# Kernel tuning notes

Hardware: AMD Instinct MI355X
Metric: run time of the kernel (lower is better)

The kernel has to match this reference:

```python
import jax, jax.numpy as jnp
import numpy as np

B, C, H, W, L, R = 1, 32, 96, 128, 2, 3
N = 2 * R + 1
EPS = 1e-5


def conv2d(x, w, stride=1, pad=1):
    return jax.lax.conv_general_dilated(
        x, w, (stride, stride), ((pad, pad), (pad, pad)),
        dimension_numbers=('NCHW', 'OIHW', 'NCHW'))


def conv_transpose2d(x, w, stride=2, pad=1):
    # torch ConvTranspose2d semantics; w: [Cin, Cout, kH, kW]
    kh, kw = w.shape[2], w.shape[3]
    wf = jnp.flip(w, (2, 3)).transpose(1, 0, 2, 3)  # [Cout, Cin, kh, kw]
    return jax.lax.conv_general_dilated(
        x, wf, (1, 1),
        ((kh - 1 - pad, kh - 1 - pad), (kw - 1 - pad, kw - 1 - pad)),
        lhs_dilation=(stride, stride),
        dimension_numbers=('NCHW', 'OIHW', 'NCHW'))


def bnorm(x, s, b, m, v):
    # inference-mode BatchNorm2d (fixed running stats)
    inv = s * jax.lax.rsqrt(v + EPS)
    return x * inv[None, :, None, None] + (b - m * inv)[None, :, None, None]


def grid_sample(img, grid):
    # bilinear, align_corners=True, padding_mode='zeros'
    # img [B,C,H,W], grid [B,Hg,Wg,2] (x,y) in [-1,1]
    Bi, Ci, Hi, Wi = img.shape
    gx = (grid[..., 0] + 1.0) * 0.5 * (Wi - 1)
    gy = (grid[..., 1] + 1.0) * 0.5 * (Hi - 1)
    x0 = jnp.floor(gx)
    y0 = jnp.floor(gy)
    wx = (gx - x0)[:, None]  # [B,1,Hg,Wg]
    wy = (gy - y0)[:, None]

    def tap(yf, xf):
        valid = (xf >= 0) & (xf <= Wi - 1) & (yf >= 0) & (yf <= Hi - 1)
        xc = jnp.clip(xf, 0, Wi - 1).astype(jnp.int32)
        yc = jnp.clip(yf, 0, Hi - 1).astype(jnp.int32)
        v = jax.vmap(lambda im, y, x: im[:, y, x])(img, yc, xc)  # [B,C,Hg,Wg]
        return v * valid[:, None].astype(img.dtype)

    v00 = tap(y0, x0)
    v01 = tap(y0, x0 + 1)
    v10 = tap(y0 + 1, x0)
    v11 = tap(y0 + 1, x0 + 1)
    return (v00 * (1 - wx) * (1 - wy) + v01 * wx * (1 - wy)
            + v10 * (1 - wx) * wy + v11 * wx * wy)


def _forward(fmap1_0, fmap1_1, fmap2_0, fmap2_1, coords,
             cw1, cw2, cw3, cw4, ctw5, cw6, cb6,
             bn1s, bn1b, bn1m, bn1v, bn2s, bn2b, bn2m, bn2v,
             bn3s, bn3b, bn3m, bn3v, bn4s, bn4b, bn4m, bn4v,
             bn5s, bn5b, bn5m, bn5v, dap_w):
    n = N
    dx = jnp.linspace(-R, R, n)
    delta = jnp.stack(jnp.meshgrid(dx, dx, indexing='ij'), axis=-1)  # [n,n,2]
    b, _, h, w = coords.shape
    cp = coords.transpose(0, 2, 3, 1)  # [b,h,w,2] (x,y)
    bns = ((bn1s, bn1b, bn1m, bn1v), (bn2s, bn2b, bn2m, bn2v),
           (bn3s, bn3b, bn3m, bn3v), (bn4s, bn4b, bn4m, bn4v),
           (bn5s, bn5b, bn5m, bn5v))
    out = []
    for i, (f1, f2) in enumerate(((fmap1_0, fmap2_0), (fmap1_1, fmap2_1))):
        c, h2, w2 = f1.shape[1], f1.shape[2], f1.shape[3]
        # [b,n,h,n,w,2]: first n axis pairs with h, second with w (as in torch view)
        cent = cp[:, None, :, None, :, :] / (2.0 ** i) + delta[None, :, None, :, None, :]
        gx = 2.0 * cent[..., 0] / (w2 - 1) - 1.0
        gy = 2.0 * cent[..., 1] / (h2 - 1) - 1.0
        grid = jnp.stack([gx, gy], -1).reshape(b, n * h, n * w, 2)
        f2s = grid_sample(f2, grid).reshape(b, c, n, h, n, w)
        f2s = f2s.transpose(0, 2, 4, 1, 3, 5)  # [b,du,dv,c,h,w]
        f1e = jnp.broadcast_to(f1[:, None, None], (b, n, n, c, h, w))
        x = jnp.concatenate([f1e, f2s], axis=3).reshape(b * n * n, 2 * c, h, w)
        # MatchingNet (DICL): conv-bn-relu stack, stride-2 down + transposed up
        x = jax.nn.relu(bnorm(conv2d(x, cw1[i]), *(p[i] for p in bns[0])))
        x = jax.nn.relu(bnorm(conv2d(x, cw2[i], stride=2), *(p[i] for p in bns[1])))
        x = jax.nn.relu(bnorm(conv2d(x, cw3[i]), *(p[i] for p in bns[2])))
        x = jax.nn.relu(bnorm(conv2d(x, cw4[i]), *(p[i] for p in bns[3])))
        x = jax.nn.relu(bnorm(conv_transpose2d(x, ctw5[i]), *(p[i] for p in bns[4])))
        x = conv2d(x, cw6[i]) + cb6[i][None, :, None, None]  # [b*n*n,1,h,w]
        cost = x.reshape(b, n * n, h, w)
        # DisplacementAwareProjection: 1x1 conv over the 49 displacement channels
        cost = jnp.einsum('pq,bqhw->bphw', dap_w[i], cost)
        out.append(cost)
    return jnp.concatenate(out, axis=1)  # [b, L*(2r+1)^2, h, w]


def setup_inputs():
    key = jax.random.key(0)
    ks = jax.random.split(key, 40)

    def rn(k, shape, scale=1.0):
        return jax.random.normal(k, shape, jnp.float32) * scale

    inp = {}
    inp['fmap1_0'] = rn(ks[0], (B, C, H, W))
    inp['fmap2_0'] = rn(ks[1], (B, C, H, W))
    inp['fmap1_1'] = rn(ks[2], (B, C, H, W))
    inp['fmap2_1'] = rn(ks[3], (B, C, H, W))
    gy, gx = jnp.meshgrid(jnp.arange(H, dtype=jnp.float32),
                          jnp.arange(W, dtype=jnp.float32), indexing='ij')
    base = jnp.stack([gx, gy], 0)[None]  # [1,2,H,W] (x,y) pixel coords
    inp['coords'] = base + rn(ks[4], (B, 2, H, W), 2.0)

    def cw(k, co, ci, kk):
        return rn(k, (L, co, ci, kk, kk), 1.0 / np.sqrt(ci * kk * kk))

    inp['cw1'] = cw(ks[5], 96, 2 * C, 3)
    inp['cw2'] = cw(ks[6], 128, 96, 3)
    inp['cw3'] = cw(ks[7], 128, 128, 3)
    inp['cw4'] = cw(ks[8], 64, 128, 3)
    inp['ctw5'] = rn(ks[9], (L, 64, 32, 4, 4), 1.0 / np.sqrt(64 * 16))
    inp['cw6'] = cw(ks[10], 1, 32, 3)
    inp['cb6'] = rn(ks[11], (L, 1), 0.1)
    for j, ch in enumerate((96, 128, 128, 64, 32), start=1):
        k4 = jax.random.split(ks[11 + j], 4)
        inp['bn%ds' % j] = 1.0 + rn(k4[0], (L, ch), 0.1)
        inp['bn%db' % j] = rn(k4[1], (L, ch), 0.1)
        inp['bn%dm' % j] = rn(k4[2], (L, ch), 0.1)
        inp['bn%dv' % j] = 1.0 + rn(k4[3], (L, ch), 0.1) ** 2
    # DAP identity init
    inp['dap_w'] = jnp.tile(jnp.eye(N * N, dtype=jnp.float32)[None], (L, 1, 1))
    return inp


def reference(fmap1_0, fmap1_1, fmap2_0, fmap2_1, coords,
              cw1, cw2, cw3, cw4, ctw5, cw6, cb6,
              bn1s, bn1b, bn1m, bn1v, bn2s, bn2b, bn2m, bn2v,
              bn3s, bn3b, bn3m, bn3v, bn4s, bn4b, bn4m, bn4v,
              bn5s, bn5b, bn5m, bn5v, dap_w):
    return _forward(fmap1_0, fmap1_1, fmap2_0, fmap2_1, coords,
                    cw1, cw2, cw3, cw4, ctw5, cw6, cb6,
                    bn1s, bn1b, bn1m, bn1v, bn2s, bn2b, bn2m, bn2v,
                    bn3s, bn3b, bn3m, bn3v, bn4s, bn4b, bn4m, bn4v,
                    bn5s, bn5b, bn5m, bn5v, dap_w)
```

## Files before the change

### kernel.cpp

```cpp
#include <hip/hip_runtime.h>

#define EPSF 1e-5f

typedef __attribute__((ext_vector_type(8))) short short8;
typedef __attribute__((ext_vector_type(4))) float f32x4;

__device__ __forceinline__ ushort f2bf(float x) {
    union { float f; unsigned u; } c; c.f = x;
    unsigned r = c.u + 0x7FFF + ((c.u >> 16) & 1);
    return (ushort)(r >> 16);
}
__device__ __forceinline__ float bf2f(ushort b) {
    union { unsigned u; float f; } c; c.u = ((unsigned)b) << 16;
    return c.f;
}
__device__ __forceinline__ int swz(int a) {
    return a ^ (((a >> 7) & 7) << 4);
}


__global__ __launch_bounds__(256) void k_repack_conv(
    const float* __restrict__ src, ushort* __restrict__ dst, int CO, int CI)
{
    int idx = blockIdx.x * 256 + threadIdx.x;
    if (idx >= CO * CI * 9) return;
    int co = idx / (CI * 9);
    int rem = idx % (CI * 9);
    int ci = rem / 9, tap = rem % 9;
    dst[((size_t)tap * CO + co) * CI + ci] = f2bf(src[idx]);
}

__global__ __launch_bounds__(256) void k_repack_ct(
    const float* __restrict__ src, ushort* __restrict__ dst)
{
    int idx = blockIdx.x * 256 + threadIdx.x;
    if (idx >= 4 * 4 * 32 * 64) return;
    int ci = idx & 63;
    int t = idx >> 6;
    int co = t & 31; t >>= 5;
    int tap = t & 3;
    int parity = t >> 2;
    int ph = parity >> 1, pw = parity & 1;
    int a = tap >> 1, b = tap & 1;
    int kh = ((ph + 1) & 1) + 2 * a;
    int kw = ((pw + 1) & 1) + 2 * b;
    dst[idx] = f2bf(src[((ci * 32 + co) * 4 + kh) * 4 + kw]);
}

__global__ __launch_bounds__(256) void k_pack_f1(
    const float* __restrict__ f1_0, const float* __restrict__ f1_1,
    ushort* __restrict__ xf1)
{
    const int sp = blockIdx.x * 256 + threadIdx.x;
    const int l = blockIdx.z;
    const float* f1 = l ? f1_1 : f1_0;
    ushort* dst = xf1 + (size_t)l * 393216 + (size_t)sp * 32;
    #pragma unroll
    for (int g = 0; g < 4; ++g) {
        uint4 pk;
        uint* pw_ = (uint*)&pk;
        #pragma unroll
        for (int q = 0; q < 4; ++q) {
            int c = g * 8 + q * 2;
            pw_[q] = (uint)f2bf(f1[(size_t)c * 12288 + sp])
                   | ((uint)f2bf(f1[(size_t)(c + 1) * 12288 + sp]) << 16);
        }
        *(uint4*)(dst + g * 8) = pk;
    }
}

__global__ __launch_bounds__(256) void k_sample_nhwc(
    const float* __restrict__ f2_0, const float* __restrict__ f2_1,
    const float* __restrict__ coords, ushort* __restrict__ x0s, int d0)
{
    const int HW = 12288;
    const int sp = blockIdx.x * 256 + threadIdx.x;
    const int slot = blockIdx.z;
    const int p = d0 + slot;
    const int l = p / 49;
    const int d = p - l * 49;
    const int du = d / 7, dv = d % 7;
    const float inv_scale = l ? 0.5f : 1.0f;
    const float* f2 = l ? f2_1 : f2_0;

    float cx = coords[sp] * inv_scale + (float)(du - 3);
    float cy = coords[HW + sp] * inv_scale + (float)(dv - 3);
    float xf = floorf(cx), yf = floorf(cy);
    float wx = cx - xf, wy = cy - yf;
    int xi = (int)xf, yi = (int)yf;
    float vx0 = (xf >= 0.f && xf <= 127.f) ? 1.f : 0.f;
    float vx1 = (xf + 1.f >= 0.f && xf + 1.f <= 127.f) ? 1.f : 0.f;
    float vy0 = (yf >= 0.f && yf <= 95.f) ? 1.f : 0.f;
    float vy1 = (yf + 1.f >= 0.f && yf + 1.f <= 95.f) ? 1.f : 0.f;
    int x0i = min(max(xi, 0), 127), x1i = min(max(xi + 1, 0), 127);
    int y0i = min(max(yi, 0), 95),  y1i = min(max(yi + 1, 0), 95);
    float w00 = (1.f - wx) * (1.f - wy) * vx0 * vy0;
    float w01 = wx * (1.f - wy) * vx1 * vy0;
    float w10 = (1.f - wx) * wy * vx0 * vy1;
    float w11 = wx * wy * vx1 * vy1;
    int o00 = y0i * 128 + x0i, o01 = y0i * 128 + x1i;
    int o10 = y1i * 128 + x0i, o11 = y1i * 128 + x1i;

    ushort* dst = x0s + ((size_t)slot * HW + sp) * 32;
    #pragma unroll
    for (int g = 0; g < 4; ++g) {
        uint4 pk;
        uint* pw_ = (uint*)&pk;
        #pragma unroll
        for (int q = 0; q < 4; ++q) {
            uint wv = 0;
            #pragma unroll
            for (int h = 0; h < 2; ++h) {
                int c = g * 8 + q * 2 + h;
                const float* fc = f2 + (size_t)c * HW;
                float s = w00 * fc[o00] + w01 * fc[o01] + w10 * fc[o10] + w11 * fc[o11];
                wv |= ((uint)f2bf(s)) << (16 * h);
            }
            pw_[q] = wv;
        }
        *(uint4*)(dst + g * 8) = pk;
    }
}

template <int EPI>
__global__ __launch_bounds__(512, 2) void k_conv1(
    const ushort* __restrict__ in,
    ushort* __restrict__ out,
    const ushort* __restrict__ wbase,
    const float* __restrict__ p1,
    const float* __restrict__ bs0, const float* __restrict__ bb0,
    const float* __restrict__ bm0, const float* __restrict__ bv0,
    int d0, int koff)
{
    constexpr int AB = 10 * 66 * 64;
    constexpr int PB = 3 * 48 * 64;
    constexpr int SA = 6;
    __shared__ __align__(16) char smem[AB + 2 * PB];
    char* As = smem;

    const int tid = threadIdx.x;
    const int lane = tid & 63, wid = tid >> 6;
    const int lr = lane & 15, kg = lane >> 4;
    const int bx = blockIdx.x;
    const int rt = bx >> 1, ct = bx & 1;
    const int r0 = rt * 8, c0 = ct * 64;
    const int y = blockIdx.y;
    const int co0 = y * 48;
    const int slot = blockIdx.z;
    const int l = EPI ? slot : (d0 + slot) / 49;

    const ushort* ib = in + (size_t)slot * 12288 * 32;
    const ushort* wl = wbase + (size_t)l * (9 * 96 * 64);
    const short8 z8 = {0, 0, 0, 0, 0, 0, 0, 0};

    #pragma unroll
    for (int i = 0; i < SA; ++i) {
        int lin = i * 8192 + tid * 16;
        if (lin < AB) {
            int pos = lin >> 6;
            int prow = (pos * 994) >> 16;
            int pcol = pos - prow * 66;
            int grow = r0 - 1 + prow, gcol = c0 - 1 + pcol;
            bool ok = ((unsigned)grow < 96u) && ((unsigned)gcol < 128u);
            short8 v = z8;
            if (ok) v = *(const short8*)(ib + (grow * 128 + gcol) * 32 + ((lin & 63) >> 1));
            *(short8*)(As + swz(lin)) = v;
        }
    }

    int boff[2]; unsigned bmask = 0;
    #pragma unroll
    for (int i = 0; i < 2; ++i) {
        int lin = i * 8192 + tid * 16;
        if (lin < PB) bmask |= 1u << i;
        int lc = min(lin, PB - 16);
        int rowidx = lc >> 6;
        int tpg = rowidx / 48;
        int r = rowidx - tpg * 48;
        boff[i] = (tpg * 96 + co0 + r) * 64 + koff + ((lc & 63) >> 1);
    }
    short8 stgB[2];
    auto loadB = [&](int pg) {
        const ushort* src = wl + pg * (3 * 96 * 64);
        #pragma unroll
        for (int i = 0; i < 2; ++i)
            if ((bmask >> i) & 1) stgB[i] = *(const short8*)(src + boff[i]);
    };
    auto writeB = [&](int pg) {
        char* Bs = smem + AB + (pg & 1) * PB;
        #pragma unroll
        for (int i = 0; i < 2; ++i) {
            int lin = i * 8192 + tid * 16;
            if ((bmask >> i) & 1) *(short8*)(Bs + swz(lin)) = stgB[i];
        }
    };

    f32x4 acc[4][3];
    if constexpr (EPI == 0) {
        const float* pl = p1 + (size_t)l * 1179648
                        + ((size_t)((bx * 2 + y) * 512 + tid)) * 48;
        #pragma unroll
        for (int mf = 0; mf < 4; ++mf)
            #pragma unroll
            for (int nf = 0; nf < 3; ++nf)
                acc[mf][nf] = *(const f32x4*)(pl + (mf * 3 + nf) * 4);
    } else {
        #pragma unroll
        for (int mf = 0; mf < 4; ++mf)
            #pragma unroll
            for (int nf = 0; nf < 3; ++nf)
                acc[mf][nf] = (f32x4){0.f, 0.f, 0.f, 0.f};
    }

    loadB(0);
    writeB(0);
    __syncthreads();

    #pragma unroll
    for (int ps = 0; ps < 3; ++ps) {
        if (ps < 2) loadB(ps + 1);
        const char* Bs = smem + AB + (ps & 1) * PB;
        #pragma unroll
        for (int kw = 0; kw < 3; ++kw) {
            short8 a[4];
            #pragma unroll
            for (int mf = 0; mf < 4; ++mf) {
                int sp = (wid + ps) * 66 + mf * 16 + lr + kw;
                a[mf] = *(const short8*)(As + swz(sp * 64 + kg * 16));
            }
            #pragma unroll
            for (int nf = 0; nf < 3; ++nf) {
                short8 b = *(const short8*)(Bs + swz((kw * 48 + nf * 16 + lr) * 64 + kg * 16));
                #pragma unroll
                for (int mf = 0; mf < 4; ++mf)
                    acc[mf][nf] = __builtin_amdgcn_mfma_f32_16x16x32_bf16(
                        a[mf], b, acc[mf][nf], 0, 0, 0);
            }
        }
        __syncthreads();
        if (ps < 2) { writeB(ps + 1); __syncthreads(); }
    }

    if constexpr (EPI == 1) {
        float* of = (float*)out + (size_t)l * 1179648
                  + ((size_t)((bx * 2 + y) * 512 + tid)) * 48;
        #pragma unroll
        for (int mf = 0; mf < 4; ++mf)
            #pragma unroll
            for (int nf = 0; nf < 3; ++nf)
                *(f32x4*)(of + (mf * 3 + nf) * 4) = acc[mf][nf];
    } else {
        const float* bs = bs0 + l * 96;
        const float* bb = bb0 + l * 96;
        const float* bm = bm0 + l * 96;
        const float* bv = bv0 + l * 96;
        ushort* ob = out + (size_t)slot * 12288 * 96;
        const int orow = r0 + wid;
        #pragma unroll
        for (int nf = 0; nf < 3; ++nf) {
            const int col = co0 + nf * 16 + lr;
            const float inv = bs[col] * rsqrtf(bv[col] + EPSF);
            const float beta = bb[col] - bm[col] * inv;
            #pragma unroll
            for (int mf = 0; mf < 4; ++mf) {
                #pragma unroll
                for (int j = 0; j < 4; ++j) {
                    int ocol = c0 + mf * 16 + kg * 4 + j;
                    float yv = fmaxf(fmaf(acc[mf][nf][j], inv, beta), 0.f);
                    ob[((size_t)orow * 128 + ocol) * 96 + col] = f2bf(yv);
                }
            }
        }
    }
}

template <int CIN, int COUT, int IH, int IW>
__global__ __launch_bounds__(512, 4) void k_conv_lds8s(
    const ushort* __restrict__ in, ushort* __restrict__ out,
    const ushort* __restrict__ wbase, int wlstride,
    const float* __restrict__ bs0, const float* __restrict__ bb0,
    const float* __restrict__ bm0, const float* __restrict__ bv0, int d0)
{
    constexpr int CCs = CIN / 32;
    constexpr int AB = 10 * 66 * 64;
    constexpr int PB = 3 * 64 * 64;
    constexpr int SA = 6, SB = 2;
    constexpr int NPH = 3 * CCs;
    __shared__ __align__(16) char smem[AB + 2 * PB];
    char* As = smem;

    const int tid = threadIdx.x;
    const int lane = tid & 63, wid = tid >> 6;
    const int lr = lane & 15, kg = lane >> 4;
    const int r0 = (int)blockIdx.x * 8;
    const int co0 = (int)blockIdx.y * 64;
    const int slot = blockIdx.z;
    const int l = (d0 + slot) / 49;

    int aoff[SA]; unsigned awr = 0, avalid = 0;
    #pragma unroll
    for (int i = 0; i < SA; ++i) {
        int lin = i * 8192 + tid * 16;
        bool wr = lin < AB;
        int linc = wr ? lin : 0;
        int pos = linc >> 6;
        int prow = (pos * 994) >> 16;
        int pcol = pos - prow * 66;
        int grow = r0 - 1 + prow, gcol = pcol - 1;
        bool ok = wr && ((unsigned)grow < (unsigned)IH) && ((unsigned)gcol < (unsigned)IW);
        if (wr) awr |= 1u << i;
        if (ok) avalid |= 1u << i;
        int growc = min(max(grow, 0), IH - 1), gcolc = min(max(gcol, 0), IW - 1);
        aoff[i] = (growc * IW + gcolc) * CIN + ((linc & 63) >> 1);
    }
    int boff[SB]; unsigned bmask = 0;
    #pragma unroll
    for (int i = 0; i < SB; ++i) {
        int lin = i * 8192 + tid * 16;
        if (lin < PB) bmask |= 1u << i;
        int lc = min(lin, PB - 16);
        int rowidx = lc >> 6;
        int tpg = rowidx >> 6, r = rowidx & 63;
        boff[i] = (tpg * COUT + co0 + r) * CIN + ((lc & 63) >> 1);
    }

    const ushort* ib = in + (size_t)slot * IH * IW * CIN;
    const ushort* wl = wbase + (size_t)l * wlstride;
    const short8 z8 = {0, 0, 0, 0, 0, 0, 0, 0};

    auto stageA = [&](int cc) {
        #pragma unroll
        for (int i = 0; i < SA; ++i) {
            int lin = i * 8192 + tid * 16;
            if ((awr >> i) & 1) {
                short8 v = z8;
                if ((avalid >> i) & 1)
                    v = *(const short8*)(ib + aoff[i] + cc * 32);
                *(short8*)(As + swz(lin)) = v;
            }
        }
    };
    short8 stgB[SB];
    auto loadB = [&](int ps) {
        int pg = ps % 3, cc = ps / 3;
        const ushort* src = wl + pg * (3 * COUT * CIN) + cc * 32;
        #pragma unroll
        for (int i = 0; i < SB; ++i)
            if ((bmask >> i) & 1) stgB[i] = *(const short8*)(src + boff[i]);
    };
    auto writeB = [&](int ps) {
        char* Bs = smem + AB + (ps & 1) * PB;
        #pragma unroll
        for (int i = 0; i < SB; ++i) {
            int lin = i * 8192 + tid * 16;
            if ((bmask >> i) & 1) *(short8*)(Bs + swz(lin)) = stgB[i];
        }
    };

    f32x4 acc[4][4];
    #pragma unroll
    for (int mf = 0; mf < 4; ++mf)
        #pragma unroll
        for (int nf = 0; nf < 4; ++nf)
            acc[mf][nf] = (f32x4){0.f, 0.f, 0.f, 0.f};

    stageA(0);
    loadB(0); writeB(0);
    __syncthreads();

    #pragma unroll 1
    for (int ps = 0; ps < NPH; ++ps) {
        const int pg = ps % 3;
        const bool hasNext = (ps + 1 < NPH);
        if (hasNext) loadB(ps + 1);

        const char* Bs = smem + AB + (ps & 1) * PB;
        #pragma unroll
        for (int kw = 0; kw < 3; ++kw) {
            short8 a[4];
            #pragma unroll
            for (int mf = 0; mf < 4; ++mf) {
                int sp = (wid + pg) * 66 + mf * 16 + lr + kw;
                a[mf] = *(const short8*)(As + swz(sp * 64 + kg * 16));
            }
            #pragma unroll
            for (int nf = 0; nf < 4; ++nf) {
                short8 b = *(const short8*)(Bs + swz((kw * 64 + nf * 16 + lr) * 64 + kg * 16));
                #pragma unroll
                for (int mf = 0; mf < 4; ++mf)
                    acc[mf][nf] = __builtin_amdgcn_mfma_f32_16x16x32_bf16(
                        a[mf], b, acc[mf][nf], 0, 0, 0);
            }
        }

        __syncthreads();
        if (hasNext) {
            writeB(ps + 1);
            if (pg == 2) stageA(ps / 3 + 1);
            __syncthreads();
        }
    }

    const float* bs = bs0 + l * COUT;
    const float* bb = bb0 + l * COUT;
    const float* bm = bm0 + l * COUT;
    const float* bv = bv0 + l * COUT;
    ushort* ob = out + (size_t)slot * IH * IW * COUT;
    const int orow = r0 + wid;
    #pragma unroll
    for (int nf = 0; nf < 4; ++nf) {
        const int col = co0 + nf * 16 + lr;
        const float inv = bs[col] * rsqrtf(bv[col] + EPSF);
        const float beta = bb[col] - bm[col] * inv;
        #pragma unroll
        for (int mf = 0; mf < 4; ++mf) {
            #pragma unroll
            for (int j = 0; j < 4; ++j) {
                int ocol = mf * 16 + kg * 4 + j;
                float y = fmaxf(fmaf(acc[mf][nf][j], inv, beta), 0.f);
                ob[((size_t)orow * IW + ocol) * COUT + col] = f2bf(y);
            }
        }
    }
}

__global__ __launch_bounds__(512, 2) void k_conv_s2_8(
    const ushort* __restrict__ in, ushort* __restrict__ out,
    const ushort* __restrict__ wbase, int wlstride,
    const float* __restrict__ bs0, const float* __restrict__ bb0,
    const float* __restrict__ bm0, const float* __restrict__ bv0, int d0)
{
    constexpr int AB = 9 * 66 * 64;
    constexpr int PB = 3 * 64 * 64;
    constexpr int SA = 5;
    constexpr int SB = 2;
    constexpr int NPH = 9;
    __shared__ __align__(16) char smem[AB + 2 * PB];
    char* As = smem;

    const int tid = threadIdx.x;
    const int lane = tid & 63, wid = tid >> 6;
    const int lr = lane & 15, kg = lane >> 4;
    const int mw = wid >> 1, ch = wid & 1;
    const int bx = blockIdx.x;
    const int rt = bx >> 1, ct = bx & 1;
    const int r0 = rt * 4, oc0 = ct * 32;
    const int co0 = blockIdx.y * 64;
    const int slot = blockIdx.z;
    const int l = (d0 + slot) / 49;

    int aoff[SA]; unsigned awr = 0, avalid = 0;
    #pragma unroll
    for (int i = 0; i < SA; ++i) {
        int lin = i * 8192 + tid * 16;
        bool wr = lin < AB;
        int linc = wr ? lin : 0;
        int pos = linc >> 6;
        int prow = (pos * 994) >> 16;
        int pcol = pos - prow * 66;
        int grow = 2 * r0 - 1 + prow, gcol = 2 * oc0 - 1 + pcol;
        bool ok = wr && ((unsigned)grow < 96u) && ((unsigned)gcol < 128u);
        if (wr) awr |= 1u << i;
        if (ok) avalid |= 1u << i;
        int growc = min(max(grow, 0), 95), gcolc = min(max(gcol, 0), 127);
        aoff[i] = (growc * 128 + gcolc) * 96 + ((linc & 63) >> 1);
    }
    int boff[SB]; unsigned bmask = 0;
    #pragma unroll
    for (int i = 0; i < SB; ++i) {
        int lin = i * 8192 + tid * 16;
        if (lin < PB) bmask |= 1u << i;
        int lc = min(lin, PB - 16);
        int rowidx = lc >> 6;
        int tpg = rowidx >> 6, r = rowidx & 63;
        boff[i] = (tpg * 128 + co0 + r) * 96 + ((lc & 63) >> 1);
    }

    const ushort* ib = in + (size_t)slot * 12288 * 96;
    const ushort* wl = wbase + (size_t)l * wlstride;
    const short8 z8 = {0, 0, 0, 0, 0, 0, 0, 0};

    short8 stgA[SA], stgB[SB];
    auto loadA = [&](int cc) {
        #pragma unroll
        for (int i = 0; i < SA; ++i) {
            if ((avalid >> i) & 1) stgA[i] = *(const short8*)(ib + aoff[i] + cc * 32);
            else stgA[i] = z8;
        }
    };
    auto writeA = [&]() {
        #pragma unroll
        for (int i = 0; i < SA; ++i) {
            int lin = i * 8192 + tid * 16;
            if ((awr >> i) & 1)
                *(short8*)(As + swz(lin)) = stgA[i];
        }
    };
    auto loadB = [&](int ps) {
        int pg = ps % 3, cc = ps / 3;
        const ushort* src = wl + pg * (3 * 128 * 96) + cc * 32;
        #pragma unroll
        for (int i = 0; i < SB; ++i)
            if ((bmask >> i) & 1) stgB[i] = *(const short8*)(src + boff[i]);
    };
    auto writeB = [&](int ps) {
        char* Bs = smem + AB + (ps & 1) * PB;
        #pragma unroll
        for (int i = 0; i < SB; ++i) {
            int lin = i * 8192 + tid * 16;
            if ((bmask >> i) & 1)
                *(short8*)(Bs + swz(lin)) = stgB[i];
        }
    };

    f32x4 acc[2][2];
    #pragma unroll
    for (int mf = 0; mf < 2; ++mf)
        #pragma unroll
        for (int nf = 0; nf < 2; ++nf)
            acc[mf][nf] = (f32x4){0.f, 0.f, 0.f, 0.f};

    loadA(0); loadB(0);
    writeA(); writeB(0);
    __syncthreads();

    #pragma unroll 1
    for (int ps = 0; ps < NPH; ++ps) {
        const int pg = ps % 3;
        const bool hasNext = (ps + 1 < NPH);
        const bool newA = (pg == 2) && hasNext;
        if (hasNext) loadB(ps + 1);
        if (newA) loadA(ps / 3 + 1);

        const char* Bs = smem + AB + (ps & 1) * PB;
        #pragma unroll
        for (int kw = 0; kw < 3; ++kw) {
            short8 a[2];
            #pragma unroll
            for (int mf = 0; mf < 2; ++mf) {
                int pos = (2 * mw + pg) * 66 + 2 * (mf * 16 + lr) + kw;
                a[mf] = *(const short8*)(As + swz(pos * 64 + kg * 16));
            }
            #pragma unroll
            for (int nf = 0; nf < 2; ++nf) {
                int rb = kw * 64 + ch * 32 + nf * 16 + lr;
                short8 b = *(const short8*)(Bs + swz(rb * 64 + kg * 16));
                #pragma unroll
                for (int mf = 0; mf < 2; ++mf)
                    acc[mf][nf] = __builtin_amdgcn_mfma_f32_16x16x32_bf16(
                        a[mf], b, acc[mf][nf], 0, 0, 0);
            }
        }

        __syncthreads();
        if (hasNext) writeB(ps + 1);
        if (newA) writeA();
        if (hasNext) __syncthreads();
    }

    const float* bs = bs0 + l * 128;
    const float* bb = bb0 + l * 128;
    const float* bm = bm0 + l * 128;
    const float* bv = bv0 + l * 128;
    ushort* ob = out + (size_t)slot * 3072 * 128;
    const int orow = r0 + mw;
    #pragma unroll
    for (int nf = 0; nf < 2; ++nf) {
        const int col = co0 + ch * 32 + nf * 16 + lr;
        const float inv = bs[col] * rsqrtf(bv[col] + EPSF);
        const float beta = bb[col] - bm[col] * inv;
        #pragma unroll
        for (int mf = 0; mf < 2; ++mf) {
            #pragma unroll
            for (int j = 0; j < 4; ++j) {
                int ocol = oc0 + mf * 16 + kg * 4 + j;
                float y = fmaxf(fmaf(acc[mf][nf][j], inv, beta), 0.f);
                ob[((size_t)orow * 64 + ocol) * 128 + col] = f2bf(y);
            }
        }
    }
}

__global__ __launch_bounds__(256) void k_convt_mfma(
    const ushort* __restrict__ in, ushort* __restrict__ out,
    const ushort* __restrict__ wbase,
    const float* __restrict__ bs0, const float* __restrict__ bb0,
    const float* __restrict__ bm0, const float* __restrict__ bv0, int d0)
{
    constexpr int SLICE = 4 * 32 * 128;
    constexpr int S = 4;
    __shared__ __align__(16) char smem[SLICE];

    const int tid = threadIdx.x;
    const int lane = tid & 63, wid = tid >> 6;
    const int lr = lane & 15, kg = lane >> 4;
    const int m0 = blockIdx.x * 256 + wid * 64;
    const int parity = blockIdx.y;
    const int slot = blockIdx.z;
    const int l = (d0 + slot) / 49;
    const int ph = parity >> 1, pw = parity & 1;
    const int kh0 = (ph + 1) & 1, kw0 = (pw + 1) & 1;

    {
        const char* wsrc = (const char*)(wbase + (size_t)l * (16 * 32 * 64));
        #pragma unroll
        for (int i = 0; i < S; ++i) {
            int lin = i * 4096 + tid * 16;
            int rowidx = lin >> 7;
            int tap = rowidx >> 5, r = rowidx & 31;
            short8 v = *(const short8*)(wsrc
                + (((size_t)(parity * 4 + tap) * 32 + r) * 64) * 2 + (lin & 127));
            *(short8*)(smem + swz(lin)) = v;
        }
    }
    __syncthreads();

    int ihA[4], iwA[4];
    #pragma unroll
    for (int mf = 0; mf < 4; ++mf) {
        int m = m0 + mf * 16 + lr;
        int q = m >> 6, r = m & 63;
        ihA[mf] = (2 * q + ph + 1 - kh0) >> 1;
        iwA[mf] = (2 * r + pw + 1 - kw0) >> 1;
    }
    const ushort* ib = in + (size_t)slot * 3072 * 64;

    const short8 z8 = {0, 0, 0, 0, 0, 0, 0, 0};
    f32x4 acc[4][2];
    #pragma unroll
    for (int mf = 0; mf < 4; ++mf)
        #pragma unroll
        for (int nf = 0; nf < 2; ++nf)
            acc[mf][nf] = (f32x4){0.f, 0.f, 0.f, 0.f};

    #pragma unroll
    for (int a = 0; a < 2; ++a) {
        #pragma unroll
        for (int b2 = 0; b2 < 2; ++b2) {
            int srcoff[4]; bool val[4];
            #pragma unroll
            for (int mf = 0; mf < 4; ++mf) {
                int ih = ihA[mf] - a;
                int iw = iwA[mf] - b2;
                val[mf] = ((unsigned)ih < 48u) && ((unsigned)iw < 64u);
                int ihc = min(max(ih, 0), 47), iwc = min(max(iw, 0), 63);
                srcoff[mf] = (ihc * 64 + iwc) * 64;
            }
            const int tap = a * 2 + b2;
            #pragma unroll
            for (int cc = 0; cc < 2; ++cc) {
                const int kbase = cc * 32 + kg * 8;
                short8 av[4];
                #pragma unroll
                for (int mf = 0; mf < 4; ++mf) {
                    short8 v = *(const short8*)(ib + srcoff[mf] + kbase);
                    av[mf] = val[mf] ? v : z8;
                }
                #pragma unroll
                for (int nf = 0; nf < 2; ++nf) {
                    short8 bfr = *(const short8*)(smem
                        + swz((tap * 32 + nf * 16 + lr) * 128 + cc * 64 + kg * 16));
                    #pragma unroll
                    for (int mf = 0; mf < 4; ++mf)
                        acc[mf][nf] = __builtin_amdgcn_mfma_f32_16x16x32_bf16(
                            av[mf], bfr, acc[mf][nf], 0, 0, 0);
                }
            }
        }
    }

    const float* bs = bs0 + l * 32;
    const float* bb = bb0 + l * 32;
    const float* bm = bm0 + l * 32;
    const float* bv = bv0 + l * 32;
    ushort* ob = out + (size_t)slot * 12288 * 32;
    #pragma unroll
    for (int nf = 0; nf < 2; ++nf) {
        const int col = nf * 16 + lr;
        const float inv = bs[col] * rsqrtf(bv[col] + EPSF);
        const float beta = bb[col] - bm[col] * inv;
        #pragma unroll
        for (int mf = 0; mf < 4; ++mf) {
            #pragma unroll
            for (int j = 0; j < 4; ++j) {
                int m = m0 + mf * 16 + kg * 4 + j;
                int q = m >> 6, r = m & 63;
                int sp = (2 * q + ph) * 128 + (2 * r + pw);
                float y = fmaxf(fmaf(acc[mf][nf][j], inv, beta), 0.f);
                ob[(size_t)sp * 32 + col] = f2bf(y);
            }
        }
    }
}

__global__ __launch_bounds__(256) void k_conv6(
    const ushort* __restrict__ x5, float* __restrict__ cost,
    const float* __restrict__ w0, const float* __restrict__ cb6, int d0)
{
    const int sp = blockIdx.x * 256 + threadIdx.x;
    const int slot = blockIdx.z;
    const int p = d0 + slot;
    const int l = p / 49;
    const float* w = w0 + l * 288;
    const int oh = sp >> 7, ow = sp & 127;
    float acc = 0.f;
    #pragma unroll
    for (int kh = 0; kh < 3; ++kh) {
        const int ih = oh - 1 + kh;
        if (ih < 0 || ih >= 96) continue;
        #pragma unroll
        for (int kw = 0; kw < 3; ++kw) {
            const int iw = ow - 1 + kw;
            if (iw < 0 || iw >= 128) continue;
            const ushort* q = x5 + ((size_t)slot * 12288 + ih * 128 + iw) * 32;
            const int tap = kh * 3 + kw;
            #pragma unroll
            for (int g = 0; g < 4; ++g) {
                uint4 v = *(const uint4*)(q + g * 8);
                const uint* vw = (const uint*)&v;
                #pragma unroll
                for (int t = 0; t < 4; ++t) {
                    int ci = g * 8 + t * 2;
                    acc = fmaf(bf2f((ushort)(vw[t] & 0xFFFF)), w[ci * 9 + tap], acc);
                    acc = fmaf(bf2f((ushort)(vw[t] >> 16)), w[(ci + 1) * 9 + tap], acc);
                }
            }
        }
    }
    cost[(size_t)p * 12288 + sp] = acc + cb6[l];
}

__global__ __launch_bounds__(256) void k_dap(
    const float* __restrict__ cost, const float* __restrict__ dw,
    float* __restrict__ out)
{
    const int sp = blockIdx.x * 256 + threadIdx.x;
    const int p = blockIdx.y;
    const float* dr = dw + p * 49;
    float acc = 0.f;
    #pragma unroll
    for (int q = 0; q < 49; ++q)
        acc = fmaf(dr[q], cost[(size_t)q * 12288 + sp], acc);
    out[(size_t)p * 12288 + sp] = acc;
}

extern "C" void kernel_launch(void* const* d_in, const int* in_sizes, int n_in,
                              void* d_out, int out_size, void* d_ws, size_t ws_size,
                              hipStream_t stream)
{
    const float* fm1_0 = (const float*)d_in[0];
    const float* fm2_0 = (const float*)d_in[1];
    const float* fm1_1 = (const float*)d_in[2];
    const float* fm2_1 = (const float*)d_in[3];
    const float* coords = (const float*)d_in[4];
    const float* cw1  = (const float*)d_in[5];
    const float* cw2  = (const float*)d_in[6];
    const float* cw3  = (const float*)d_in[7];
    const float* cw4  = (const float*)d_in[8];
    const float* ctw5 = (const float*)d_in[9];
    const float* cw6  = (const float*)d_in[10];
    const float* cb6  = (const float*)d_in[11];
    const float* bn[5][4];
    for (int j = 0; j < 5; ++j)
        for (int k = 0; k < 4; ++k)
            bn[j][k] = (const float*)d_in[12 + j * 4 + k];
    const float* dap = (const float*)d_in[32];
    float* out = (float*)d_out;

    const size_t A_US = 393216;
    const size_t B_US = 1179648;
    const size_t XF1 = 2 * 393216;
    const size_t W1 = 9 * 96 * 64, W2 = 9 * 128 * 96, W3 = 9 * 128 * 128;
    const size_t W4 = 9 * 64 * 128, W5 = 16 * 32 * 64;
    const size_t W_US = 2 * (W1 + W2 + W3 + W4 + W5);
    const size_t P1F = 2 * (size_t)24 * 2 * 512 * 48;
    const size_t COSTF = (size_t)98 * 12288;

    int DC = 1;
    for (int cand : {98, 66, 49, 42, 33, 25, 17, 13, 9, 7, 5, 3, 2, 1}) {
        size_t need = (A_US + B_US) * (size_t)cand * 2 + (XF1 + W_US) * 2
                    + (P1F + COSTF) * 4 + 4096;
        if (need <= ws_size) { DC = cand; break; }
    }

    ushort* bufA = (ushort*)d_ws;
    ushort* bufB = bufA + A_US * DC;
    ushort* xf1 = bufB + B_US * DC;
    ushort* wp = xf1 + XF1;
    ushort* wr1 = wp; wp += 2 * W1;
    ushort* wr2 = wp; wp += 2 * W2;
    ushort* wr3 = wp; wp += 2 * W3;
    ushort* wr4 = wp; wp += 2 * W4;
    ushort* wr5 = wp; wp += 2 * W5;
    float* P1 = (float*)wp;
    float* cost = P1 + P1F;

    for (int l = 0; l < 2; ++l) {
        k_repack_conv<<<dim3(216), 256, 0, stream>>>(cw1 + (size_t)l * W1, wr1 + l * W1, 96, 64);
        k_repack_conv<<<dim3(432), 256, 0, stream>>>(cw2 + (size_t)l * W2, wr2 + l * W2, 128, 96);
        k_repack_conv<<<dim3(576), 256, 0, stream>>>(cw3 + (size_t)l * W3, wr3 + l * W3, 128, 128);
        k_repack_conv<<<dim3(288), 256, 0, stream>>>(cw4 + (size_t)l * W4, wr4 + l * W4, 64, 128);
        k_repack_ct<<<dim3(128), 256, 0, stream>>>(ctw5 + (size_t)l * W5, wr5 + l * W5);
    }

    k_pack_f1<<<dim3(48, 1, 2), 256, 0, stream>>>(fm1_0, fm1_1, xf1);
    k_conv1<1><<<dim3(24, 2, 2), 512, 0, stream>>>(
        xf1, (ushort*)P1, wr1, nullptr,
        bn[0][0], bn[0][1], bn[0][2], bn[0][3], 0, 0);

    for (int d0 = 0; d0 < 98; d0 += DC) {
        const int ndd = min(DC, 98 - d0);
        k_sample_nhwc<<<dim3(48, 1, ndd), 256, 0, stream>>>(
            fm2_0, fm2_1, coords, bufA, d0);
        k_conv1<0><<<dim3(24, 2, ndd), 512, 0, stream>>>(
            bufA, bufB, wr1, P1,
            bn[0][0], bn[0][1], bn[0][2], bn[0][3], d0, 32);
        k_conv_s2_8<<<dim3(24, 2, ndd), 512, 0, stream>>>(bufB, bufA, wr2, (int)W2,
                bn[1][0], bn[1][1], bn[1][2], bn[1][3], d0);
        k_conv_lds8s<128, 128, 48, 64>
            <<<dim3(6, 2, ndd), 512, 0, stream>>>(bufA, bufB, wr3, (int)W3,
                bn[2][0], bn[2][1], bn[2][2], bn[2][3], d0);
        k_conv_lds8s<128, 64, 48, 64>
            <<<dim3(6, 1, ndd), 512, 0, stream>>>(bufB, bufA, wr4, (int)W4,
                bn[3][0], bn[3][1], bn[3][2], bn[3][3], d0);
        k_convt_mfma<<<dim3(12, 4, ndd), 256, 0, stream>>>(bufA, bufB, wr5,
                bn[4][0], bn[4][1], bn[4][2], bn[4][3], d0);
        k_conv6<<<dim3(48, 1, ndd), 256, 0, stream>>>(
            bufB, cost, cw6, cb6, d0);
    }
    for (int l = 0; l < 2; ++l)
        k_dap<<<dim3(48, 49), 256, 0, stream>>>(
            cost + (size_t)l * 49 * 12288, dap + (size_t)l * 49 * 49,
            out + (size_t)l * 49 * 12288);
}
```

Baseline: 753.4 us.

## Stage transposed-conv input halo tile in LDS with double-buffered weights

Rewrites the stride-2 transposed convolution so each 512-thread block stages an 8-row input tile plus a one-pixel halo (10x66 positions, 32 channels per half) into LDS. The four taps then read the A fragment from shared memory instead of issuing four separate global gathers with bounds masks. Weights are split into two channel halves and double-buffered, with the next half prefetched into registers during compute. The block is larger and the grid is halved, so more LDS is used per block and there is an extra barrier phase between the two channel halves.

```diff
diff --git a/kernel.cpp b/kernel.cpp
--- a/kernel.cpp
+++ b/kernel.cpp
@@ -581,51 +581,76 @@
     }
 }
 
-__global__ __launch_bounds__(256) void k_convt_mfma(
+__global__ __launch_bounds__(512, 4) void k_convt_lds(
     const ushort* __restrict__ in, ushort* __restrict__ out,
     const ushort* __restrict__ wbase,
     const float* __restrict__ bs0, const float* __restrict__ bb0,
     const float* __restrict__ bm0, const float* __restrict__ bv0, int d0)
 {
-    constexpr int SLICE = 4 * 32 * 128;
-    constexpr int S = 4;
-    __shared__ __align__(16) char smem[SLICE];
+    constexpr int AB = 10 * 66 * 64;
+    constexpr int PB = 4 * 32 * 64;
+    constexpr int SA = 6;
+    __shared__ __align__(16) char smem[AB + 2 * PB];
+    char* As = smem;
 
     const int tid = threadIdx.x;
     const int lane = tid & 63, wid = tid >> 6;
     const int lr = lane & 15, kg = lane >> 4;
-    const int m0 = blockIdx.x * 256 + wid * 64;
+    const int q0 = (int)blockIdx.x * 8;
     const int parity = blockIdx.y;
+    const int ph = parity >> 1, pw = parity & 1;
     const int slot = blockIdx.z;
     const int l = (d0 + slot) / 49;
-    const int ph = parity >> 1, pw = parity & 1;
-    const int kh0 = (ph + 1) & 1, kw0 = (pw + 1) & 1;
-
+
+    int aoff[SA]; unsigned awr = 0, avalid = 0;
+    #pragma unroll
+    for (int i = 0; i < SA; ++i) {
+        int lin = i * 8192 + tid * 16;
+        bool wr = lin < AB;
+        int linc = wr ? lin : 0;
+        int pos = linc >> 6;
+        int prow = (pos * 994) >> 16;
+        int pcol = pos - prow * 66;
+        int grow = q0 - 1 + prow, gcol = pcol - 1;
+        bool ok = wr && ((unsigned)grow < 48u) && ((unsigned)gcol < 64u);
+        if (wr) awr |= 1u << i;
+        if (ok) avalid |= 1u << i;
+        int growc = min(max(grow, 0), 47), gcolc = min(max(gcol, 0), 63);
+        aoff[i] = (growc * 64 + gcolc) * 64 + ((linc & 63) >> 1);
+    }
+    int boffB;
     {
-        const char* wsrc = (const char*)(wbase + (size_t)l * (16 * 32 * 64));
-        #pragma unroll
-        for (int i = 0; i < S; ++i) {
-            int lin = i * 4096 + tid * 16;
-            int rowidx = lin >> 7;
-            int tap = rowidx >> 5, r = rowidx & 31;
-            short8 v = *(const short8*)(wsrc
-                + (((size_t)(parity * 4 + tap) * 32 + r) * 64) * 2 + (lin & 127));
-            *(short8*)(smem + swz(lin)) = v;
-        }
-    }
-    __syncthreads();
-
-    int ihA[4], iwA[4];
-    #pragma unroll
-    for (int mf = 0; mf < 4; ++mf) {
-        int m = m0 + mf * 16 + lr;
-        int q = m >> 6, r = m & 63;
-        ihA[mf] = (2 * q + ph + 1 - kh0) >> 1;
-        iwA[mf] = (2 * r + pw + 1 - kw0) >> 1;
-    }
+        int lin = tid * 16;
+        int rowidx = lin >> 6;
+        int tap = rowidx >> 5, co = rowidx & 31;
+        boffB = ((parity * 4 + tap) * 32 + co) * 64 + ((lin & 63) >> 1);
+    }
+
     const ushort* ib = in + (size_t)slot * 3072 * 64;
-
+    const ushort* wl = wbase + (size_t)l * (16 * 32 * 64);
     const short8 z8 = {0, 0, 0, 0, 0, 0, 0, 0};
+
+    auto stageA = [&](int cc) {
+        #pragma unroll
+        for (int i = 0; i < SA; ++i) {
+            int lin = i * 8192 + tid * 16;
+            if ((awr >> i) & 1) {
+                short8 v = z8;
+                if ((avalid >> i) & 1)
+                    v = *(const short8*)(ib + aoff[i] + cc * 32);
+                *(short8*)(As + swz(lin)) = v;
+            }
+        }
+    };
+    short8 stgB;
+    auto loadB = [&](int cc) {
+        stgB = *(const short8*)(wl + boffB + cc * 32);
+    };
+    auto writeB = [&](int cc) {
+        char* Bs = smem + AB + (cc & 1) * PB;
+        *(short8*)(Bs + swz(tid * 16)) = stgB;
+    };
+
     f32x4 acc[4][2];
     #pragma unroll
     for (int mf = 0; mf < 4; ++mf)
@@ -633,39 +658,41 @@
         for (int nf = 0; nf < 2; ++nf)
             acc[mf][nf] = (f32x4){0.f, 0.f, 0.f, 0.f};
 
-    #pragma unroll
-    for (int a = 0; a < 2; ++a) {
-        #pragma unroll
-        for (int b2 = 0; b2 < 2; ++b2) {
-            int srcoff[4]; bool val[4];
-            #pragma unroll
-            for (int mf = 0; mf < 4; ++mf) {
-                int ih = ihA[mf] - a;
-                int iw = iwA[mf] - b2;
-                val[mf] = ((unsigned)ih < 48u) && ((unsigned)iw < 64u);
-                int ihc = min(max(ih, 0), 47), iwc = min(max(iw, 0), 63);
-                srcoff[mf] = (ihc * 64 + iwc) * 64;
-            }
-            const int tap = a * 2 + b2;
-            #pragma unroll
-            for (int cc = 0; cc < 2; ++cc) {
-                const int kbase = cc * 32 + kg * 8;
+    stageA(0);
+    loadB(0); writeB(0);
+    __syncthreads();
+
+    #pragma unroll 1
+    for (int cc = 0; cc < 2; ++cc) {
+        if (cc == 0) loadB(1);
+        const char* Bs = smem + AB + (cc & 1) * PB;
+        #pragma unroll
+        for (int a = 0; a < 2; ++a) {
+            #pragma unroll
+            for (int b2 = 0; b2 < 2; ++b2) {
+                const int tap = a * 2 + b2;
                 short8 av[4];
                 #pragma unroll
                 for (int mf = 0; mf < 4; ++mf) {
-                    short8 v = *(const short8*)(ib + srcoff[mf] + kbase);
-                    av[mf] = val[mf] ? v : z8;
+                    int pos = (wid + 1 + ph - a) * 66 + mf * 16 + lr + pw - b2 + 1;
+                    av[mf] = *(const short8*)(As + swz(pos * 64 + kg * 16));
                 }
                 #pragma unroll
                 for (int nf = 0; nf < 2; ++nf) {
-                    short8 bfr = *(const short8*)(smem
-                        + swz((tap * 32 + nf * 16 + lr) * 128 + cc * 64 + kg * 16));
+                    short8 b = *(const short8*)(Bs
+                        + swz((tap * 32 + nf * 16 + lr) * 64 + kg * 16));
                     #pragma unroll
                     for (int mf = 0; mf < 4; ++mf)
                         acc[mf][nf] = __builtin_amdgcn_mfma_f32_16x16x32_bf16(
-                            av[mf], bfr, acc[mf][nf], 0, 0, 0);
+                            av[mf], b, acc[mf][nf], 0, 0, 0);
                 }
             }
+        }
+        __syncthreads();
+        if (cc == 0) {
+            writeB(1);
+            stageA(1);
+            __syncthreads();
         }
     }
 
@@ -674,6 +701,7 @@
     const float* bm = bm0 + l * 32;
     const float* bv = bv0 + l * 32;
     ushort* ob = out + (size_t)slot * 12288 * 32;
+    const size_t rowb = (size_t)(2 * (q0 + wid) + ph) * 128;
     #pragma unroll
     for (int nf = 0; nf < 2; ++nf) {
         const int col = nf * 16 + lr;
@@ -683,11 +711,9 @@
         for (int mf = 0; mf < 4; ++mf) {
             #pragma unroll
             for (int j = 0; j < 4; ++j) {
-                int m = m0 + mf * 16 + kg * 4 + j;
-                int q = m >> 6, r = m & 63;
-                int sp = (2 * q + ph) * 128 + (2 * r + pw);
+                int r = mf * 16 + kg * 4 + j;
                 float y = fmaxf(fmaf(acc[mf][nf][j], inv, beta), 0.f);
-                ob[(size_t)sp * 32 + col] = f2bf(y);
+                ob[(rowb + 2 * r + pw) * 32 + col] = f2bf(y);
             }
         }
     }
@@ -823,7 +849,7 @@
         k_conv_lds8s<128, 64, 48, 64>
             <<<dim3(6, 1, ndd), 512, 0, stream>>>(bufB, bufA, wr4, (int)W4,
                 bn[3][0], bn[3][1], bn[3][2], bn[3][3], d0);
-        k_convt_mfma<<<dim3(12, 4, ndd), 256, 0, stream>>>(bufA, bufB, wr5,
+        k_convt_lds<<<dim3(6, 4, ndd), 512, 0, stream>>>(bufA, bufB, wr5,
                 bn[4][0], bn[4][1], bn[4][2], bn[4][3], d0);
         k_conv6<<<dim3(48, 1, ndd), 256, 0, stream>>>(
             bufB, cost, cw6, cb6, d0);
```

Measured after the change: 735.8 us. 1.02x faster.
